# Kernel optimization log

Measured on AMD Instinct MI355X. Metric: run time of the kernel, lower is better.

## Reference

```python
import jax, jax.numpy as jnp
import numpy as np

K = 3          # kernel size (both dims)
PAD = 1        # padding used both for offset_mask conv and deform_conv2d
KK = K * K


def setup_inputs() -> dict:
    key = jax.random.key(0)
    k0, k1, k2, k3, k4 = jax.random.split(key, 5)
    B, C, H, W, O = 8, 64, 64, 64, 64
    input_feat = jax.random.normal(k0, (B, C, H, W), jnp.float32)
    degrad_inter = jax.random.normal(k1, (B, C, H, W), jnp.float32)
    stdv = 1.0 / np.sqrt(C * K * K)
    weight = jax.random.uniform(k2, (O, C, K, K), jnp.float32, -stdv, stdv)
    # small-magnitude offset/mask conv params -> realistic small learned offsets
    om_weight = jax.random.normal(k3, (3 * KK, 2 * C, K, K), jnp.float32) * 0.01
    om_bias = jax.random.normal(k4, (3 * KK,), jnp.float32) * 0.01
    return {"input_feat": input_feat, "degrad_inter": degrad_inter,
            "weight": weight, "om_weight": om_weight, "om_bias": om_bias}


def _conv2d(x, w, b):
    out = jax.lax.conv_general_dilated(
        x, w, window_strides=(1, 1), padding=((PAD, PAD), (PAD, PAD)),
        dimension_numbers=("NCHW", "OIHW", "NCHW"))
    return out + b[None, :, None, None]


def _deform_conv2d(x, offset, mask, weight):
    # x: (B,C,H,W); offset: (B,2*KK,H,W) with channel 2k=dy_k, 2k+1=dx_k;
    # mask: (B,KK,H,W); weight: (O,C,K,K). stride=1, padding=PAD, dilation=1.
    B, C, H, W = x.shape
    O = weight.shape[0]
    off = offset.reshape(B, KK, 2, H, W)
    dy, dx = off[:, :, 0], off[:, :, 1]                       # (B,KK,H,W)

    ky, kx = jnp.meshgrid(jnp.arange(K), jnp.arange(K), indexing="ij")
    ky = ky.reshape(KK).astype(x.dtype)
    kx = kx.reshape(KK).astype(x.dtype)
    hh = jnp.arange(H, dtype=x.dtype)
    ww = jnp.arange(W, dtype=x.dtype)
    # absolute fractional sample locations: (B,KK,H,W)
    y = hh[None, None, :, None] - PAD + ky[None, :, None, None] + dy
    xq = ww[None, None, None, :] - PAD + kx[None, :, None, None] + dx

    y0 = jnp.floor(y).astype(jnp.int32)
    x0 = jnp.floor(xq).astype(jnp.int32)
    y1, x1 = y0 + 1, x0 + 1
    wy = y - y0.astype(x.dtype)
    wx = xq - x0.astype(x.dtype)

    x_flat = x.reshape(B, C, H * W)

    def gather(yi, xi):
        valid = (yi >= 0) & (yi < H) & (xi >= 0) & (xi < W)
        idx = jnp.clip(yi, 0, H - 1) * W + jnp.clip(xi, 0, W - 1)  # (B,KK,H,W)
        vals = jax.vmap(lambda im, ix: im[:, ix])(x_flat, idx)     # (B,C,KK,H,W)
        return vals * valid[:, None].astype(x.dtype)

    wy_ = wy[:, None]  # (B,1,KK,H,W)
    wx_ = wx[:, None]
    sampled = (gather(y0, x0) * (1 - wy_) * (1 - wx_)
               + gather(y0, x1) * (1 - wy_) * wx_
               + gather(y1, x0) * wy_ * (1 - wx_)
               + gather(y1, x1) * wy_ * wx_)                       # (B,C,KK,H,W)
    sampled = sampled * mask[:, None]
    return jnp.einsum("bckhw,ock->bohw", sampled, weight.reshape(O, C, KK))


def reference(input_feat, degrad_inter, weight, om_weight, om_bias):
    concat = jnp.concatenate([input_feat, degrad_inter], axis=1)
    om = _conv2d(concat, om_weight, om_bias)                       # (B,3*KK,H,W)
    off1, off2, mask = jnp.split(om, 3, axis=1)
    offset = jnp.concatenate([off1, off2], axis=1)                 # (B,2*KK,H,W)
    mask = jax.nn.sigmoid(mask)                                    # (B,KK,H,W)
    return _deform_conv2d(input_feat, offset, mask, weight)
```

## Files before the change

### kernel.cpp

```cpp
#include <hip/hip_runtime.h>
#include <math.h>

#define WO_PK_OFF 36864
#define CATT_OFF  73728

typedef short  short8  __attribute__((ext_vector_type(8)));
typedef float  float4v __attribute__((ext_vector_type(4)));

static __device__ __forceinline__ short f2bf(float f) {
    unsigned int u = __builtin_bit_cast(unsigned int, f);
    u += 0x7FFFu + ((u >> 16) & 1u);
    return (short)(u >> 16);
}
static __device__ __forceinline__ float bf2f(unsigned short u) {
    return __builtin_bit_cast(float, (unsigned int)u << 16);
}

__global__ __launch_bounds__(256) void prep_transpose(
    const float* __restrict__ feat, const float* __restrict__ deg,
    const float* __restrict__ weight, const float* __restrict__ om_weight,
    unsigned short* __restrict__ catT,
    short* __restrict__ wd_pk, short* __restrict__ wo_pk)
{
    __shared__ unsigned short T[64 * 136];
    const int tid = threadIdx.x;
    if (blockIdx.x < 512) {
        const int b = blockIdx.x >> 6, h = blockIdx.x & 63;
        const int lane = tid & 63, wv = tid >> 6;
#pragma unroll
        for (int cc = 0; cc < 32; cc++) {
            int c = wv * 32 + cc;
            const float* src = (c < 64)
                ? (feat + (size_t)(b * 64 + c) * 4096)
                : (deg  + (size_t)(b * 64 + (c - 64)) * 4096);
            T[lane * 136 + c] = (unsigned short)f2bf(src[h * 64 + lane]);
        }
        __syncthreads();
        const int px = tid >> 2, seg = tid & 3;
        unsigned short* dst =
            catT + (size_t)(b * 4096 + h * 64 + px) * 128 + seg * 32;
#pragma unroll
        for (int j = 0; j < 4; j++)
            *(uint4*)(dst + j * 8) = *(const uint4*)&T[px * 136 + seg * 32 + j * 8];
    } else {
        int idx = (blockIdx.x - 512) * 256 + tid;
        if (idx < 36864) {
            int j = idx & 7, o = (idx >> 3) & 63;
            int lq = (idx >> 9) & 3, ks = idx >> 11;
            int t = ks >> 1, c = (ks & 1) * 32 + lq * 8 + j;
            wd_pk[idx] = f2bf(weight[(o * 64 + c) * 9 + t]);
        } else {
            int e = idx - 36864;
            int j = e & 7, oc = (e >> 3) & 31;
            int lq = (e >> 8) & 3, ks2 = e >> 10;
            int quarter = ks2 / 9, t = ks2 - quarter * 9;
            int cg = quarter * 32 + lq * 8 + j;
            wo_pk[e] = (oc < 27) ? f2bf(om_weight[(oc * 128 + cg) * 9 + t])
                                 : (short)0;
        }
    }
}

__global__ __launch_bounds__(256, 2) void fused_kernel(
    const unsigned short* __restrict__ catT, const short* __restrict__ wd_pk,
    const short* __restrict__ wo_pk, const float* __restrict__ om_bias,
    float* __restrict__ out)
{
    __shared__ float T[4 * 576];
    const int tid = threadIdx.x;
    const int lane = tid & 63, wv = tid >> 6;
    const int l16 = lane & 15, lq = lane >> 4;
    const int gw = blockIdx.x * 4 + wv;
    const int b = gw >> 8, tile = gw & 255;
    const int h = tile >> 2, w0 = (tile & 3) << 4;
    const int pxx = w0 + l16;
    const unsigned short* cb = catT + (size_t)b * 4096 * 128;
    const short8 zf = {0, 0, 0, 0, 0, 0, 0, 0};

    auto loadB1 = [&](int s) -> short8 {
        int quarter = s / 9, t = s - quarter * 9;
        int ky = t / 3, kx = t - ky * 3;
        int yy = h - 1 + ky, xx = pxx - 1 + kx;
        bool ok = (yy >= 0) & (yy <= 63) & (xx >= 0) & (xx <= 63);
        int yc = min(max(yy, 0), 63), xc = min(max(xx, 0), 63);
        short8 v = *(const short8*)(cb + (yc * 64 + xc) * 128
                                       + quarter * 32 + lq * 8);
        return ok ? v : zf;
    };
    auto loadA1 = [&](int s, int m) -> short8 {
        return *(const short8*)(wo_pk + (size_t)(s * 4 + lq) * 256
                                      + (m * 16 + l16) * 8);
    };
    float4v oacc0 = {0.f, 0.f, 0.f, 0.f};
    float4v oacc1 = {0.f, 0.f, 0.f, 0.f};
    short8 bC = loadB1(0), a0C = loadA1(0, 0), a1C = loadA1(0, 1);
#pragma unroll
    for (int s = 0; s < 36; s++) {
        short8 bN = zf, a0N = zf, a1N = zf;
        if (s + 1 < 36) {
            bN  = loadB1(s + 1);
            a0N = loadA1(s + 1, 0);
            a1N = loadA1(s + 1, 1);
        }
        oacc0 = __builtin_amdgcn_mfma_f32_16x16x32_bf16(a0C, bC, oacc0, 0, 0, 0);
        oacc1 = __builtin_amdgcn_mfma_f32_16x16x32_bf16(a1C, bC, oacc1, 0, 0, 0);
        bC = bN; a0C = a0N; a1C = a1N;
    }

    float* Tw = T + wv * 576;
#pragma unroll
    for (int r = 0; r < 4; r++) {
        Tw[l16 * 36 + lq * 4 + r]      = oacc0[r];
        Tw[l16 * 36 + 16 + lq * 4 + r] = oacc1[r];
    }
    __syncthreads();
    float omv[28];
#pragma unroll
    for (int jj = 0; jj < 7; jj++) {
        float4v tv = *(const float4v*)&Tw[l16 * 36 + jj * 4];
        omv[jj * 4 + 0] = tv[0]; omv[jj * 4 + 1] = tv[1];
        omv[jj * 4 + 2] = tv[2]; omv[jj * 4 + 3] = tv[3];
    }
#pragma unroll
    for (int j = 0; j < 27; j++) omv[j] += om_bias[j];

    float4v acc0 = {0.f, 0.f, 0.f, 0.f}, acc1 = {0.f, 0.f, 0.f, 0.f};
    float4v acc2 = {0.f, 0.f, 0.f, 0.f}, acc3 = {0.f, 0.f, 0.f, 0.f};
#pragma unroll
    for (int t = 0; t < 9; t++) {
        const int ky = t / 3, kx = t - ky * 3;
        float dy = omv[2 * t], dx = omv[2 * t + 1];
        float mm = 1.f / (1.f + __expf(-omv[18 + t]));
        float yf = (float)(h - 1 + ky) + dy;
        float xf = (float)(pxx - 1 + kx) + dx;
        float fy = floorf(yf), fx = floorf(xf);
        int y0 = (int)fy, x0 = (int)fx;
        float wy = yf - fy, wx = xf - fx;
        bool vy0 = (y0 >= 0) & (y0 < 64);
        bool vy1 = (y0 >= -1) & (y0 < 63);
        bool vx0 = (x0 >= 0) & (x0 < 64);
        bool vx1 = (x0 >= -1) & (x0 < 63);
        float a0 = (1.f - wy) * mm, a1 = wy * mm;
        float W00 = a0 * (1.f - wx) * (float)(vy0 & vx0);
        float W01 = a0 * wx         * (float)(vy0 & vx1);
        float W10 = a1 * (1.f - wx) * (float)(vy1 & vx0);
        float W11 = a1 * wx         * (float)(vy1 & vx1);
        int iy0 = min(max(y0, 0), 63),     ix0 = min(max(x0, 0), 63);
        int iy1 = min(max(y0 + 1, 0), 63), ix1 = min(max(x0 + 1, 0), 63);
        const unsigned short* p00 = cb + (iy0 * 64 + ix0) * 128 + lq * 8;
        const unsigned short* p01 = cb + (iy0 * 64 + ix1) * 128 + lq * 8;
        const unsigned short* p10 = cb + (iy1 * 64 + ix0) * 128 + lq * 8;
        const unsigned short* p11 = cb + (iy1 * 64 + ix1) * 128 + lq * 8;
        short8 c00a = *(const short8*)p00,        c01a = *(const short8*)p01;
        short8 c10a = *(const short8*)p10,        c11a = *(const short8*)p11;
        short8 c00b = *(const short8*)(p00 + 32), c01b = *(const short8*)(p01 + 32);
        short8 c10b = *(const short8*)(p10 + 32), c11b = *(const short8*)(p11 + 32);
        const short* D0 = wd_pk + (size_t)((2 * t) * 4 + lq) * 512;
        const short* D1 = wd_pk + (size_t)((2 * t + 1) * 4 + lq) * 512;
        short8 d00 = *(const short8*)(D0 + l16 * 8);
        short8 d01 = *(const short8*)(D0 + (16 + l16) * 8);
        short8 d02 = *(const short8*)(D0 + (32 + l16) * 8);
        short8 d03 = *(const short8*)(D0 + (48 + l16) * 8);
        short8 d10 = *(const short8*)(D1 + l16 * 8);
        short8 d11 = *(const short8*)(D1 + (16 + l16) * 8);
        short8 d12 = *(const short8*)(D1 + (32 + l16) * 8);
        short8 d13 = *(const short8*)(D1 + (48 + l16) * 8);
        short8 bfr0, bfr1;
#pragma unroll
        for (int j = 0; j < 8; j++) {
            float v0 = W00 * bf2f((unsigned short)c00a[j])
                     + W01 * bf2f((unsigned short)c01a[j])
                     + W10 * bf2f((unsigned short)c10a[j])
                     + W11 * bf2f((unsigned short)c11a[j]);
            float v1 = W00 * bf2f((unsigned short)c00b[j])
                     + W01 * bf2f((unsigned short)c01b[j])
                     + W10 * bf2f((unsigned short)c10b[j])
                     + W11 * bf2f((unsigned short)c11b[j]);
            bfr0[j] = f2bf(v0);
            bfr1[j] = f2bf(v1);
        }
        acc0 = __builtin_amdgcn_mfma_f32_16x16x32_bf16(d00, bfr0, acc0, 0, 0, 0);
        acc1 = __builtin_amdgcn_mfma_f32_16x16x32_bf16(d01, bfr0, acc1, 0, 0, 0);
        acc2 = __builtin_amdgcn_mfma_f32_16x16x32_bf16(d02, bfr0, acc2, 0, 0, 0);
        acc3 = __builtin_amdgcn_mfma_f32_16x16x32_bf16(d03, bfr0, acc3, 0, 0, 0);
        acc0 = __builtin_amdgcn_mfma_f32_16x16x32_bf16(d10, bfr1, acc0, 0, 0, 0);
        acc1 = __builtin_amdgcn_mfma_f32_16x16x32_bf16(d11, bfr1, acc1, 0, 0, 0);
        acc2 = __builtin_amdgcn_mfma_f32_16x16x32_bf16(d12, bfr1, acc2, 0, 0, 0);
        acc3 = __builtin_amdgcn_mfma_f32_16x16x32_bf16(d13, bfr1, acc3, 0, 0, 0);
    }

    float* ob = out + (size_t)(b * 64) * 4096 + h * 64 + w0 + l16;
#pragma unroll
    for (int r = 0; r < 4; r++) ob[(lq * 4 + r) * 4096]      = acc0[r];
#pragma unroll
    for (int r = 0; r < 4; r++) ob[(16 + lq * 4 + r) * 4096] = acc1[r];
#pragma unroll
    for (int r = 0; r < 4; r++) ob[(32 + lq * 4 + r) * 4096] = acc2[r];
#pragma unroll
    for (int r = 0; r < 4; r++) ob[(48 + lq * 4 + r) * 4096] = acc3[r];
}

extern "C" void kernel_launch(void* const* d_in, const int* in_sizes, int n_in,
                              void* d_out, int out_size, void* d_ws, size_t ws_size,
                              hipStream_t stream)
{
    const float* feat      = (const float*)d_in[0];
    const float* deg       = (const float*)d_in[1];
    const float* weight    = (const float*)d_in[2];
    const float* om_weight = (const float*)d_in[3];
    const float* om_bias   = (const float*)d_in[4];
    float* out = (float*)d_out;
    short* wss = (short*)d_ws;
    unsigned short* catT = (unsigned short*)(wss + CATT_OFF);

    hipLaunchKernelGGL(prep_transpose, dim3(800), dim3(256), 0, stream,
                       feat, deg, weight, om_weight, catT,
                       wss, wss + WO_PK_OFF);
    hipLaunchKernelGGL(fused_kernel,   dim3(512), dim3(256), 0, stream,
                       catT, wss, wss + WO_PK_OFF, om_bias, out);
}
```

Baseline: 119.3 us.

## Stage conv weights in LDS with double buffering, remap block to one image row

Each block now covers one full row (four 16-pixel tiles of the same batch and row) instead of four arbitrary tiles. The offset-conv and deform-conv weight fragments are cooperatively loaded into shared memory, double buffered per channel quarter and per tap, instead of each wave fetching them from global memory on its own. The goal is less redundant global and L2 weight traffic. In exchange it adds a block-wide barrier per stage and uses more LDS, which may reduce occupancy and the overlap between loads and MFMAs.

```diff
diff --git a/kernel.cpp b/kernel.cpp
--- a/kernel.cpp
+++ b/kernel.cpp
@@ -66,68 +66,105 @@
     const short* __restrict__ wo_pk, const float* __restrict__ om_bias,
     float* __restrict__ out)
 {
-    __shared__ float T[4 * 576];
+    __shared__ short8 Lraw[2304];
+    short8* A1 = Lraw;
+    float*  Tw = (float*)Lraw;
+    short8* A3 = Lraw + 576;
+
     const int tid = threadIdx.x;
     const int lane = tid & 63, wv = tid >> 6;
     const int l16 = lane & 15, lq = lane >> 4;
-    const int gw = blockIdx.x * 4 + wv;
-    const int b = gw >> 8, tile = gw & 255;
-    const int h = tile >> 2, w0 = (tile & 3) << 4;
+    const int b = blockIdx.x & 7;
+    const int h = blockIdx.x >> 3;
+    const int w0 = wv << 4;
     const int pxx = w0 + l16;
     const unsigned short* cb = catT + (size_t)b * 4096 * 128;
     const short8 zf = {0, 0, 0, 0, 0, 0, 0, 0};
 
-    auto loadB1 = [&](int s) -> short8 {
-        int quarter = s / 9, t = s - quarter * 9;
+    auto loadB1 = [&](int q, int t) -> short8 {
         int ky = t / 3, kx = t - ky * 3;
         int yy = h - 1 + ky, xx = pxx - 1 + kx;
         bool ok = (yy >= 0) & (yy <= 63) & (xx >= 0) & (xx <= 63);
         int yc = min(max(yy, 0), 63), xc = min(max(xx, 0), 63);
         short8 v = *(const short8*)(cb + (yc * 64 + xc) * 128
-                                       + quarter * 32 + lq * 8);
+                                       + q * 32 + lq * 8);
         return ok ? v : zf;
     };
-    auto loadA1 = [&](int s, int m) -> short8 {
-        return *(const short8*)(wo_pk + (size_t)(s * 4 + lq) * 256
-                                      + (m * 16 + l16) * 8);
-    };
+
+    {
+        const short8* src = (const short8*)wo_pk;
+        short8 g0 = src[tid], g1 = src[tid + 256];
+        short8 g2 = src[tid + 512], g3 = src[tid + 768];
+        short8 g4 = zf; if (tid < 128) g4 = src[tid + 1024];
+        A1[tid] = g0; A1[tid + 256] = g1; A1[tid + 512] = g2; A1[tid + 768] = g3;
+        if (tid < 128) A1[tid + 1024] = g4;
+    }
+    __syncthreads();
+
     float4v oacc0 = {0.f, 0.f, 0.f, 0.f};
     float4v oacc1 = {0.f, 0.f, 0.f, 0.f};
-    short8 bC = loadB1(0), a0C = loadA1(0, 0), a1C = loadA1(0, 1);
-#pragma unroll
-    for (int s = 0; s < 36; s++) {
-        short8 bN = zf, a0N = zf, a1N = zf;
-        if (s + 1 < 36) {
-            bN  = loadB1(s + 1);
-            a0N = loadA1(s + 1, 0);
-            a1N = loadA1(s + 1, 1);
-        }
-        oacc0 = __builtin_amdgcn_mfma_f32_16x16x32_bf16(a0C, bC, oacc0, 0, 0, 0);
-        oacc1 = __builtin_amdgcn_mfma_f32_16x16x32_bf16(a1C, bC, oacc1, 0, 0, 0);
-        bC = bN; a0C = a0N; a1C = a1N;
-    }
-
-    float* Tw = T + wv * 576;
+#pragma unroll
+    for (int q = 0; q < 4; q++) {
+        const int bufo = (q & 1) * 1152;
+        short8 g0 = zf, g1 = zf, g2 = zf, g3 = zf, g4 = zf;
+        if (q < 3) {
+            const short8* src = (const short8*)(wo_pk + (q + 1) * 9216);
+            g0 = src[tid]; g1 = src[tid + 256];
+            g2 = src[tid + 512]; g3 = src[tid + 768];
+            if (tid < 128) g4 = src[tid + 1024];
+        }
+        short8 b0 = loadB1(q, 0), b1 = loadB1(q, 1), b2 = loadB1(q, 2);
+        short8 b3 = loadB1(q, 3), b4 = loadB1(q, 4), b5 = loadB1(q, 5);
+        short8 b6 = loadB1(q, 6), b7 = loadB1(q, 7), b8 = loadB1(q, 8);
+#define PH1_STEP(SL, BREG) { \
+        short8 af0 = A1[bufo + (SL) * 128 + lq * 32 + l16]; \
+        short8 af1 = A1[bufo + (SL) * 128 + lq * 32 + 16 + l16]; \
+        oacc0 = __builtin_amdgcn_mfma_f32_16x16x32_bf16(af0, BREG, oacc0, 0, 0, 0); \
+        oacc1 = __builtin_amdgcn_mfma_f32_16x16x32_bf16(af1, BREG, oacc1, 0, 0, 0); }
+        PH1_STEP(0, b0) PH1_STEP(1, b1) PH1_STEP(2, b2)
+        PH1_STEP(3, b3) PH1_STEP(4, b4) PH1_STEP(5, b5)
+        PH1_STEP(6, b6) PH1_STEP(7, b7) PH1_STEP(8, b8)
+#undef PH1_STEP
+        if (q < 3) {
+            const int bufn = ((q + 1) & 1) * 1152;
+            A1[bufn + tid] = g0; A1[bufn + tid + 256] = g1;
+            A1[bufn + tid + 512] = g2; A1[bufn + tid + 768] = g3;
+            if (tid < 128) A1[bufn + tid + 1024] = g4;
+        }
+        __syncthreads();
+    }
+
+    float* Twv = Tw + wv * 576;
 #pragma unroll
     for (int r = 0; r < 4; r++) {
-        Tw[l16 * 36 + lq * 4 + r]      = oacc0[r];
-        Tw[l16 * 36 + 16 + lq * 4 + r] = oacc1[r];
-    }
+        Twv[l16 * 36 + lq * 4 + r]      = oacc0[r];
+        Twv[l16 * 36 + 16 + lq * 4 + r] = oacc1[r];
+    }
+    short8 s0 = ((const short8*)wd_pk)[tid];
+    short8 s1 = ((const short8*)wd_pk)[tid + 256];
     __syncthreads();
     float omv[28];
 #pragma unroll
     for (int jj = 0; jj < 7; jj++) {
-        float4v tv = *(const float4v*)&Tw[l16 * 36 + jj * 4];
+        float4v tv = *(const float4v*)&Twv[l16 * 36 + jj * 4];
         omv[jj * 4 + 0] = tv[0]; omv[jj * 4 + 1] = tv[1];
         omv[jj * 4 + 2] = tv[2]; omv[jj * 4 + 3] = tv[3];
     }
 #pragma unroll
     for (int j = 0; j < 27; j++) omv[j] += om_bias[j];
+    A3[tid] = s0; A3[tid + 256] = s1;
+    __syncthreads();
 
     float4v acc0 = {0.f, 0.f, 0.f, 0.f}, acc1 = {0.f, 0.f, 0.f, 0.f};
     float4v acc2 = {0.f, 0.f, 0.f, 0.f}, acc3 = {0.f, 0.f, 0.f, 0.f};
 #pragma unroll
     for (int t = 0; t < 9; t++) {
+        const int bo = (t & 1) * 512;
+        short8 g0 = zf, g1 = zf;
+        if (t < 8) {
+            const short8* src = (const short8*)wd_pk + (t + 1) * 512;
+            g0 = src[tid]; g1 = src[tid + 256];
+        }
         const int ky = t / 3, kx = t - ky * 3;
         float dy = omv[2 * t], dx = omv[2 * t + 1];
         float mm = 1.f / (1.f + __expf(-omv[18 + t]));
@@ -155,16 +192,14 @@
         short8 c10a = *(const short8*)p10,        c11a = *(const short8*)p11;
         short8 c00b = *(const short8*)(p00 + 32), c01b = *(const short8*)(p01 + 32);
         short8 c10b = *(const short8*)(p10 + 32), c11b = *(const short8*)(p11 + 32);
-        const short* D0 = wd_pk + (size_t)((2 * t) * 4 + lq) * 512;
-        const short* D1 = wd_pk + (size_t)((2 * t + 1) * 4 + lq) * 512;
-        short8 d00 = *(const short8*)(D0 + l16 * 8);
-        short8 d01 = *(const short8*)(D0 + (16 + l16) * 8);
-        short8 d02 = *(const short8*)(D0 + (32 + l16) * 8);
-        short8 d03 = *(const short8*)(D0 + (48 + l16) * 8);
-        short8 d10 = *(const short8*)(D1 + l16 * 8);
-        short8 d11 = *(const short8*)(D1 + (16 + l16) * 8);
-        short8 d12 = *(const short8*)(D1 + (32 + l16) * 8);
-        short8 d13 = *(const short8*)(D1 + (48 + l16) * 8);
+        short8 d00 = A3[bo + lq * 64 + l16];
+        short8 d01 = A3[bo + lq * 64 + 16 + l16];
+        short8 d02 = A3[bo + lq * 64 + 32 + l16];
+        short8 d03 = A3[bo + lq * 64 + 48 + l16];
+        short8 d10 = A3[bo + 256 + lq * 64 + l16];
+        short8 d11 = A3[bo + 256 + lq * 64 + 16 + l16];
+        short8 d12 = A3[bo + 256 + lq * 64 + 32 + l16];
+        short8 d13 = A3[bo + 256 + lq * 64 + 48 + l16];
         short8 bfr0, bfr1;
 #pragma unroll
         for (int j = 0; j < 8; j++) {
@@ -187,6 +222,11 @@
         acc1 = __builtin_amdgcn_mfma_f32_16x16x32_bf16(d11, bfr1, acc1, 0, 0, 0);
         acc2 = __builtin_amdgcn_mfma_f32_16x16x32_bf16(d12, bfr1, acc2, 0, 0, 0);
         acc3 = __builtin_amdgcn_mfma_f32_16x16x32_bf16(d13, bfr1, acc3, 0, 0, 0);
+        if (t < 8) {
+            const int bn = ((t + 1) & 1) * 512;
+            A3[bn + tid] = g0; A3[bn + tid + 256] = g1;
+        }
+        __syncthreads();
     }
 
     float* ob = out + (size_t)(b * 64) * 4096 + h * 64 + w0 + l16;
```

After: 115.6 us. 1.03x faster.
